# Kernel tuning notes

Hardware: AMD Instinct MI355X
Metric: run time of the kernel (lower is better)

Reference implementation:

```python
import jax, jax.numpy as jnp
import numpy as np

N_NODES = 100000
N_EDGES = 1000000
IN_DIM = 64
HID_DIM = 64


def _gcn_conv(x, W, b, rows, cols, deg_inv_sqrt):
    # x: [N, Fin] -> [N, Fout]; rows/cols already include self-loops
    xw = x @ W                                   # [N, Fout]
    norm = deg_inv_sqrt[rows] * deg_inv_sqrt[cols]  # [E+N]
    msg = xw[cols] * norm[:, None]               # gather + scale, [E+N, Fout]
    out = jax.ops.segment_sum(msg, rows, num_segments=x.shape[0])  # scatter-add
    return out + b


def _prelu(x, a):
    return jnp.where(x >= 0, x, a * x)


def _encode(x, edge_index, perm, W1, b1, prelu_a, W2, b2):
    N = x.shape[0]
    loops = jnp.arange(N, dtype=edge_index.dtype)
    rows = jnp.concatenate([edge_index[0], loops])
    cols = jnp.concatenate([edge_index[1], loops])
    deg = jax.ops.segment_sum(jnp.ones_like(rows, dtype=x.dtype), rows, num_segments=N)
    dis = jnp.where(deg > 0, jax.lax.rsqrt(deg), 0.0)

    def enc(feat):
        h = _gcn_conv(feat, W1, b1, rows, cols, dis)
        h = _prelu(h, prelu_a)
        return _gcn_conv(h, W2, b2, rows, cols, dis)

    positive = enc(x)
    negative = enc(x[perm])  # corruption: row permutation of features
    summary = jax.nn.sigmoid(positive.mean(axis=0))
    return positive, negative, summary


def setup_inputs() -> dict:
    key = jax.random.key(0)
    kx, ke, kp, k1, k2 = jax.random.split(key, 5)
    x = jax.random.normal(kx, (N_NODES, IN_DIM), dtype=jnp.float32)
    edge_index = jax.random.randint(ke, (2, N_EDGES), 0, N_NODES, dtype=jnp.int32)
    perm = jax.random.permutation(kp, N_NODES).astype(jnp.int32)
    s1 = 1.0 / np.sqrt(IN_DIM)
    s2 = 1.0 / np.sqrt(HID_DIM)
    W1 = jax.random.uniform(k1, (IN_DIM, HID_DIM), jnp.float32, -s1, s1)
    b1 = jnp.zeros((HID_DIM,), jnp.float32)
    W2 = jax.random.uniform(k2, (HID_DIM, HID_DIM), jnp.float32, -s2, s2)
    b2 = jnp.zeros((HID_DIM,), jnp.float32)
    prelu_a = jnp.float32(0.25)
    return {"x": x, "edge_index": edge_index, "perm": perm,
            "W1": W1, "b1": b1, "prelu_a": prelu_a, "W2": W2, "b2": b2}


def reference(x, edge_index, perm, W1, b1, prelu_a, W2, b2):
    return _encode(x, edge_index, perm, W1, b1, prelu_a, W2, b2)
```

## Files before the change

kernel.cpp:

```cpp
#include <hip/hip_runtime.h>
#include <hip/hip_fp16.h>
#include <math.h>

namespace {

constexpr int NN = 100000;
constexpr int NE = 1000000;
constexpr int D  = 64;

constexpr int RPB_LOG = 8;
constexpr int RPB = 1 << RPB_LOG;
constexpr int NBUK = (NN + RPB - 1) >> RPB_LOG;
constexpr int CAP = 4096;
constexpr int TILE = 8192;
constexpr int NTILES = (NE + TILE - 1) / TILE;
constexpr int EPT = TILE / 512;
constexpr int G1B = (NN / 16 + 7) / 8;
constexpr int SUMS = 256;

using ushort_t = unsigned short;
typedef __attribute__((ext_vector_type(8))) short short8;
typedef __attribute__((ext_vector_type(4))) float f32x4;

union FragU { uint4 v; short8 s; };

__device__ inline void split2(float f0, float f1, unsigned int& hi, unsigned int& lo) {
    unsigned int u0 = __float_as_uint(f0);
    unsigned int u1 = __float_as_uint(f1);
    hi = (u0 >> 16) | (u1 & 0xffff0000u);
    float l0 = f0 - __uint_as_float(u0 & 0xffff0000u);
    float l1 = f1 - __uint_as_float(u1 & 0xffff0000u);
    lo = (__float_as_uint(l0) >> 16) | (__float_as_uint(l1) & 0xffff0000u);
}

__device__ inline unsigned int packh(float a, float b) {
    union { __half2 h; unsigned int u; } cv;
    cv.h = __float22half2_rn(make_float2(a, b));
    return cv.u;
}

__device__ inline float2 h2f(unsigned int v) {
    union { unsigned int u; __half2 h; } cv;
    cv.u = v;
    return __half22float2(cv.h);
}

__device__ inline void build_wfrags(const float* __restrict__ W, int lane,
                                    FragU (&whi)[4][2], FragU (&wlo)[4][2]) {
#pragma unroll
    for (int ft = 0; ft < 4; ++ft) {
#pragma unroll
        for (int kt = 0; kt < 2; ++kt) {
            int m  = ft * 16 + (lane & 15);
            int k0 = kt * 32 + (lane >> 4) * 8;
            unsigned int hi0, lo0, hi1, lo1, hi2, lo2, hi3, lo3;
            split2(W[(k0 + 0) * 64 + m], W[(k0 + 1) * 64 + m], hi0, lo0);
            split2(W[(k0 + 2) * 64 + m], W[(k0 + 3) * 64 + m], hi1, lo1);
            split2(W[(k0 + 4) * 64 + m], W[(k0 + 5) * 64 + m], hi2, lo2);
            split2(W[(k0 + 6) * 64 + m], W[(k0 + 7) * 64 + m], hi3, lo3);
            whi[ft][kt].v = make_uint4(hi0, hi1, hi2, hi3);
            wlo[ft][kt].v = make_uint4(lo0, lo1, lo2, lo3);
        }
    }
}

__global__ void pre_k(const int* __restrict__ rows, const int* __restrict__ cols,
                      int* __restrict__ bcount, unsigned int* __restrict__ binned, int e,
                      const float* __restrict__ W1,
                      const float* __restrict__ x, const int* __restrict__ perm,
                      ushort_t* __restrict__ tPN) {
    __shared__ int gbase[NBUK];
    __shared__ int lofs[NBUK];
    int bid = blockIdx.x;

    if (bid >= NTILES) {
        int lane  = threadIdx.x & 63;
        int wtile = (bid - NTILES) * 8 + (threadIdx.x >> 6);
        if (wtile * 16 >= NN) return;
        int node = wtile * 16 + (lane & 15);
        int kg   = lane >> 4;

        FragU whi[4][2];
        FragU wlo[4][2];
        build_wfrags(W1, lane, whi, wlo);

        const float4* xr = (const float4*)x;
        size_t rbase = (size_t)node * 16 + (size_t)(kg * 2);
        int pnode = perm[node];
        size_t pbase = (size_t)pnode * 16 + (size_t)(kg * 2);
        f32x4 accP[4];
        f32x4 accN[4];
#pragma unroll
        for (int ft = 0; ft < 4; ++ft) {
            accP[ft] = f32x4{0.f, 0.f, 0.f, 0.f};
            accN[ft] = f32x4{0.f, 0.f, 0.f, 0.f};
        }
#pragma unroll
        for (int kt = 0; kt < 2; ++kt) {
            float4 a0 = xr[rbase + kt * 8];
            float4 a1 = xr[rbase + kt * 8 + 1];
            float4 g0 = xr[pbase + kt * 8];
            float4 g1 = xr[pbase + kt * 8 + 1];
            unsigned int h0, l0, h1, l1, h2, l2, h3, l3;
            split2(a0.x, a0.y, h0, l0);
            split2(a0.z, a0.w, h1, l1);
            split2(a1.x, a1.y, h2, l2);
            split2(a1.z, a1.w, h3, l3);
            FragU xhiP, xloP;
            xhiP.v = make_uint4(h0, h1, h2, h3);
            xloP.v = make_uint4(l0, l1, l2, l3);
            split2(g0.x, g0.y, h0, l0);
            split2(g0.z, g0.w, h1, l1);
            split2(g1.x, g1.y, h2, l2);
            split2(g1.z, g1.w, h3, l3);
            FragU xhiN, xloN;
            xhiN.v = make_uint4(h0, h1, h2, h3);
            xloN.v = make_uint4(l0, l1, l2, l3);
#pragma unroll
            for (int ft = 0; ft < 4; ++ft) {
                accP[ft] = __builtin_amdgcn_mfma_f32_16x16x32_bf16(whi[ft][kt].s, xhiP.s, accP[ft], 0, 0, 0);
                accP[ft] = __builtin_amdgcn_mfma_f32_16x16x32_bf16(whi[ft][kt].s, xloP.s, accP[ft], 0, 0, 0);
                accP[ft] = __builtin_amdgcn_mfma_f32_16x16x32_bf16(wlo[ft][kt].s, xhiP.s, accP[ft], 0, 0, 0);
                accN[ft] = __builtin_amdgcn_mfma_f32_16x16x32_bf16(whi[ft][kt].s, xhiN.s, accN[ft], 0, 0, 0);
                accN[ft] = __builtin_amdgcn_mfma_f32_16x16x32_bf16(whi[ft][kt].s, xloN.s, accN[ft], 0, 0, 0);
                accN[ft] = __builtin_amdgcn_mfma_f32_16x16x32_bf16(wlo[ft][kt].s, xhiN.s, accN[ft], 0, 0, 0);
            }
        }
        int fo = kg * 4;
        ushort_t* p = tPN + (size_t)node * 128;
#pragma unroll
        for (int ft = 0; ft < 4; ++ft) {
            uint2 up = make_uint2(packh(accP[ft][0], accP[ft][1]),
                                  packh(accP[ft][2], accP[ft][3]));
            *(uint2*)(p + ft * 16 + fo) = up;
            uint2 un = make_uint2(packh(accN[ft][0], accN[ft][1]),
                                  packh(accN[ft][2], accN[ft][3]));
            *(uint2*)(p + 64 + ft * 16 + fo) = un;
        }
        return;
    }

    int base = bid * TILE;
    for (int i = threadIdx.x; i < NBUK; i += blockDim.x) {
        lofs[i] = 0;
    }
    __syncthreads();
    unsigned int v[EPT];
    int bk[EPT];
    int lx[EPT];
#pragma unroll
    for (int j = 0; j < EPT; ++j) {
        int i = base + j * 512 + (int)threadIdx.x;
        if (i < e) {
            int r = rows[i];
            int c = cols[i];
            bk[j] = r >> RPB_LOG;
            v[j] = ((unsigned int)(r & (RPB - 1)) << 17) | (unsigned int)c;
            lx[j] = atomicAdd(&lofs[bk[j]], 1);
        } else {
            bk[j] = -1;
        }
    }
    __syncthreads();
    for (int b = threadIdx.x; b < NBUK; b += blockDim.x) {
        int h = lofs[b];
        gbase[b] = h ? atomicAdd(&bcount[b], h) : 0;
    }
    __syncthreads();
#pragma unroll
    for (int j = 0; j < EPT; ++j) {
        if (bk[j] >= 0) {
            int p = gbase[bk[j]] + lx[j];
            if (p < CAP) {
                binned[(size_t)bk[j] * CAP + p] = v[j];
            }
        }
    }
}

__global__ void bucket_sort_k(const unsigned int* __restrict__ binned,
                              const int* __restrict__ bcount,
                              int* __restrict__ scols, int* __restrict__ rowstart,
                              int* __restrict__ deg, float* __restrict__ dis) {
    __shared__ int lcur[RPB];
    __shared__ int srs[RPB];
    __shared__ int wsum[8];
    __shared__ int redpart[8];
    __shared__ int sbase;
    int b = blockIdx.x;
    int row0 = b << RPB_LOG;
    int nrows = min(RPB, NN - row0);
    int cnt = bcount[b];
    const unsigned int* src = binned + (size_t)b * CAP;
    int tid = threadIdx.x;
    int lane = tid & 63;
    int wid = tid >> 6;

    int bv = (tid < NBUK && tid < b) ? bcount[tid] : 0;
    int bs = bv;
#pragma unroll
    for (int off = 1; off < 64; off <<= 1) {
        bs += __shfl_xor(bs, off, 64);
    }
    if (lane == 0) redpart[wid] = bs;
    __syncthreads();
    if (tid == 0) {
        int t = 0;
        for (int w = 0; w < 8; ++w) t += redpart[w];
        sbase = t;
    }
    if (tid < RPB) {
        lcur[tid] = 0;
    }
    __syncthreads();
    int bb = sbase;

    for (int i = tid; i < cnt; i += blockDim.x) {
        atomicAdd(&lcur[src[i] >> 17], 1);
    }
    __syncthreads();
    int d = (tid < nrows) ? lcur[tid] : 0;
    int inc = d;
#pragma unroll
    for (int off = 1; off < 64; off <<= 1) {
        int t = __shfl_up(inc, off);
        if (lane >= off) inc += t;
    }
    if (lane == 63) wsum[wid] = inc;
    __syncthreads();
    int wpre = 0;
    for (int w = 0; w < wid; ++w) wpre += wsum[w];
    int gstart = bb + wpre + inc - d;
    if (tid < nrows) {
        rowstart[row0 + tid] = gstart;
        deg[row0 + tid] = d;
        dis[row0 + tid] = rsqrtf((float)(d + 1));
    }
    __syncthreads();
    if (tid < RPB) {
        srs[tid] = gstart;
        lcur[tid] = 0;
    }
    __syncthreads();
    for (int i = tid; i < cnt; i += blockDim.x) {
        unsigned int v = src[i];
        int rl = (int)(v >> 17);
        int pos = srs[rl] + atomicAdd(&lcur[rl], 1);
        scols[pos] = (int)(v & 0x1FFFFu);
    }
}

__global__ void agg_gemm_k(const ushort_t* __restrict__ tIn, ushort_t* __restrict__ tOut,
                           const float* __restrict__ dis,
                           const int* __restrict__ rowstart, const int* __restrict__ deg,
                           const int* __restrict__ scols,
                           const float* __restrict__ bias, const float* __restrict__ prelu_a,
                           const float* __restrict__ W2) {
    __shared__ float Hs[2][16][68];
    int tid = threadIdx.x;
    int lane = tid & 63;
    int wv = tid >> 6;
    int row0 = blockIdx.x * 16;
    int hl = lane & 31;
    int half = lane >> 5;
    size_t lofs = (size_t)(half * 64 + hl * 2);
    float aPr = *prelu_a;

    for (int rr = 0; rr < 4; ++rr) {
        int r = row0 + wv * 4 + rr;
        int rs   = __builtin_amdgcn_readfirstlane(r);
        int base = __builtin_amdgcn_readfirstlane(rowstart[rs]);
        int dg   = __builtin_amdgcn_readfirstlane(deg[rs]);
        float dr = dis[rs];
        unsigned int sv = *(const unsigned int*)(tIn + (size_t)rs * 128 + lofs);
        float2 fs = h2f(sv);
        float a0 = dr * fs.x;
        float a1 = dr * fs.y;
        int j = 0;
        for (; j + 4 <= dg; j += 4) {
            int c0 = scols[base + j];
            int c1 = scols[base + j + 1];
            int c2 = scols[base + j + 2];
            int c3 = scols[base + j + 3];
            float d0 = dis[c0];
            float d1 = dis[c1];
            float d2 = dis[c2];
            float d3 = dis[c3];
            unsigned int v0 = *(const unsigned int*)(tIn + (size_t)c0 * 128 + lofs);
            unsigned int v1 = *(const unsigned int*)(tIn + (size_t)c1 * 128 + lofs);
            unsigned int v2 = *(const unsigned int*)(tIn + (size_t)c2 * 128 + lofs);
            unsigned int v3 = *(const unsigned int*)(tIn + (size_t)c3 * 128 + lofs);
            float2 f0 = h2f(v0);
            float2 f1 = h2f(v1);
            float2 f2 = h2f(v2);
            float2 f3 = h2f(v3);
            a0 = fmaf(d0, f0.x, a0);
            a1 = fmaf(d0, f0.y, a1);
            a0 = fmaf(d1, f1.x, a0);
            a1 = fmaf(d1, f1.y, a1);
            a0 = fmaf(d2, f2.x, a0);
            a1 = fmaf(d2, f2.y, a1);
            a0 = fmaf(d3, f3.x, a0);
            a1 = fmaf(d3, f3.y, a1);
        }
        for (; j < dg; ++j) {
            int c = scols[base + j];
            float dc = dis[c];
            unsigned int v = *(const unsigned int*)(tIn + (size_t)c * 128 + lofs);
            float2 f = h2f(v);
            a0 = fmaf(dc, f.x, a0);
            a1 = fmaf(dc, f.y, a1);
        }
        float2 bv = *(const float2*)(bias + 2 * hl);
        float v0 = fmaf(dr, a0, bv.x);
        float v1 = fmaf(dr, a1, bv.y);
        v0 = v0 >= 0.f ? v0 : aPr * v0;
        v1 = v1 >= 0.f ? v1 : aPr * v1;
        int rl = wv * 4 + rr;
        Hs[half][rl][2 * hl]     = v0;
        Hs[half][rl][2 * hl + 1] = v1;
    }
    __syncthreads();

    int kg = lane >> 4;
    int nd = lane & 15;
    int hsel = wv >> 1;
    int ftb = (wv & 1) * 2;
    FragU whi[2][2];
    FragU wlo[2][2];
#pragma unroll
    for (int f2 = 0; f2 < 2; ++f2) {
#pragma unroll
        for (int kt = 0; kt < 2; ++kt) {
            int m  = (ftb + f2) * 16 + (lane & 15);
            int k0 = kt * 32 + (lane >> 4) * 8;
            unsigned int hi0, lo0, hi1, lo1, hi2, lo2, hi3, lo3;
            split2(W2[(k0 + 0) * 64 + m], W2[(k0 + 1) * 64 + m], hi0, lo0);
            split2(W2[(k0 + 2) * 64 + m], W2[(k0 + 3) * 64 + m], hi1, lo1);
            split2(W2[(k0 + 4) * 64 + m], W2[(k0 + 5) * 64 + m], hi2, lo2);
            split2(W2[(k0 + 6) * 64 + m], W2[(k0 + 7) * 64 + m], hi3, lo3);
            whi[f2][kt].v = make_uint4(hi0, hi1, hi2, hi3);
            wlo[f2][kt].v = make_uint4(lo0, lo1, lo2, lo3);
        }
    }
    f32x4 acc[2];
    acc[0] = f32x4{0.f, 0.f, 0.f, 0.f};
    acc[1] = f32x4{0.f, 0.f, 0.f, 0.f};
#pragma unroll
    for (int kt = 0; kt < 2; ++kt) {
        float4 a0 = *(const float4*)&Hs[hsel][nd][kt * 32 + kg * 8];
        float4 a1 = *(const float4*)&Hs[hsel][nd][kt * 32 + kg * 8 + 4];
        unsigned int h0, l0, h1, l1, h2, l2, h3, l3;
        split2(a0.x, a0.y, h0, l0);
        split2(a0.z, a0.w, h1, l1);
        split2(a1.x, a1.y, h2, l2);
        split2(a1.z, a1.w, h3, l3);
        FragU xhi, xlo;
        xhi.v = make_uint4(h0, h1, h2, h3);
        xlo.v = make_uint4(l0, l1, l2, l3);
#pragma unroll
        for (int f2 = 0; f2 < 2; ++f2) {
            acc[f2] = __builtin_amdgcn_mfma_f32_16x16x32_bf16(whi[f2][kt].s, xhi.s, acc[f2], 0, 0, 0);
            acc[f2] = __builtin_amdgcn_mfma_f32_16x16x32_bf16(whi[f2][kt].s, xlo.s, acc[f2], 0, 0, 0);
            acc[f2] = __builtin_amdgcn_mfma_f32_16x16x32_bf16(wlo[f2][kt].s, xhi.s, acc[f2], 0, 0, 0);
        }
    }
    float s = dis[row0 + nd];
    ushort_t* p = tOut + (size_t)(row0 + nd) * 128 + hsel * 64;
    int fo = kg * 4;
#pragma unroll
    for (int f2 = 0; f2 < 2; ++f2) {
        uint2 u = make_uint2(packh(s * acc[f2][0], s * acc[f2][1]),
                             packh(s * acc[f2][2], s * acc[f2][3]));
        *(uint2*)(p + (ftb + f2) * 16 + fo) = u;
    }
}

__global__ void agg_dual_k(const ushort_t* __restrict__ tPN,
                           float* __restrict__ dstP, float* __restrict__ dstN,
                           const float* __restrict__ dis,
                           const int* __restrict__ rowstart, const int* __restrict__ deg,
                           const int* __restrict__ scols,
                           const float* __restrict__ bias,
                           float* __restrict__ acc2, int n) {
    __shared__ float red[4][64];
    int lane = threadIdx.x & 63;
    int hl = lane & 31;
    int half = lane >> 5;
    int wv = threadIdx.x >> 6;
    int r = blockIdx.x * (blockDim.x >> 6) + wv;
    float v0 = 0.f;
    float v1 = 0.f;
    if (r < n) {
        int rs   = __builtin_amdgcn_readfirstlane(r);
        int base = __builtin_amdgcn_readfirstlane(rowstart[rs]);
        int dg   = __builtin_amdgcn_readfirstlane(deg[rs]);
        float dr = dis[rs];
        size_t lofs = (size_t)(half * 64 + hl * 2);
        unsigned int sv = *(const unsigned int*)(tPN + (size_t)rs * 128 + lofs);
        float2 fs = h2f(sv);
        float a0 = fs.x;
        float a1 = fs.y;
        int j = 0;
        for (; j + 4 <= dg; j += 4) {
            int c0 = scols[base + j];
            int c1 = scols[base + j + 1];
            int c2 = scols[base + j + 2];
            int c3 = scols[base + j + 3];
            unsigned int u0 = *(const unsigned int*)(tPN + (size_t)c0 * 128 + lofs);
            unsigned int u1 = *(const unsigned int*)(tPN + (size_t)c1 * 128 + lofs);
            unsigned int u2 = *(const unsigned int*)(tPN + (size_t)c2 * 128 + lofs);
            unsigned int u3 = *(const unsigned int*)(tPN + (size_t)c3 * 128 + lofs);
            float2 f0 = h2f(u0);
            float2 f1 = h2f(u1);
            float2 f2 = h2f(u2);
            float2 f3 = h2f(u3);
            a0 += f0.x + f1.x + f2.x + f3.x;
            a1 += f0.y + f1.y + f2.y + f3.y;
        }
        for (; j < dg; ++j) {
            int c = scols[base + j];
            unsigned int u = *(const unsigned int*)(tPN + (size_t)c * 128 + lofs);
            float2 f = h2f(u);
            a0 += f.x;
            a1 += f.y;
        }
        float2 bv = *(const float2*)(bias + 2 * hl);
        v0 = fmaf(dr, a0, bv.x);
        v1 = fmaf(dr, a1, bv.y);
        float* dst = half ? dstN : dstP;
        *(float2*)(dst + (size_t)rs * D + 2 * hl) = float2{v0, v1};
    }
    if (half == 0) {
        red[wv][2 * hl]     = v0;
        red[wv][2 * hl + 1] = v1;
    }
    __syncthreads();
    if (threadIdx.x < 64) {
        float t = (red[0][threadIdx.x] + red[1][threadIdx.x]) +
                  (red[2][threadIdx.x] + red[3][threadIdx.x]);
        atomicAdd(&acc2[((blockIdx.x & (SUMS - 1)) << 6) + threadIdx.x], t);
    }
}

__global__ void summary_final_k(const float* __restrict__ acc2, float* __restrict__ out, int n) {
    __shared__ float red[4][64];
    int f = threadIdx.x & 63;
    int g = threadIdx.x >> 6;
    float t = 0.f;
#pragma unroll
    for (int k = 0; k < SUMS / 4; ++k) {
        t += acc2[((g + 4 * k) << 6) + f];
    }
    red[g][f] = t;
    __syncthreads();
    if (threadIdx.x < 64) {
        float m = (red[0][f] + red[1][f] + red[2][f] + red[3][f]) / (float)n;
        out[f] = 1.f / (1.f + expf(-m));
    }
}

}

extern "C" void kernel_launch(void* const* d_in, const int* in_sizes, int n_in,
                              void* d_out, int out_size, void* d_ws, size_t ws_size,
                              hipStream_t stream) {
    (void)in_sizes; (void)n_in; (void)out_size; (void)ws_size;
    const float* x       = (const float*)d_in[0];
    const int*   ei      = (const int*)  d_in[1];
    const int*   perm    = (const int*)  d_in[2];
    const float* W1      = (const float*)d_in[3];
    const float* b1      = (const float*)d_in[4];
    const float* prelu_a = (const float*)d_in[5];
    const float* W2      = (const float*)d_in[6];
    const float* b2      = (const float*)d_in[7];

    float* outP = (float*)d_out;
    float* outN = outP + (size_t)NN * D;
    float* outS = outN + (size_t)NN * D;

    const int* erows = ei;
    const int* ecols = ei + NE;

    char* ws = (char*)d_ws;
    size_t off = 0;
    auto alloc = [&](size_t bytes) {
        void* p = ws + off;
        off = (off + bytes + 255) & ~(size_t)255;
        return p;
    };
    int*      deg      = (int*)     alloc((size_t)NN * 4);
    float*    dis      = (float*)   alloc((size_t)NN * 4);
    int*      rowstart = (int*)     alloc((size_t)NN * 4);
    int*      bcount   = (int*)     alloc((size_t)NBUK * 4);
    float*    acc2     = (float*)   alloc((size_t)SUMS * D * 4);
    unsigned int* binned = (unsigned int*)alloc((size_t)NBUK * CAP * 4);
    int*      scols    = (int*)     alloc((size_t)NE * 4);
    ushort_t* tPN      = (ushort_t*)alloc((size_t)NN * 128 * 2);
    ushort_t* tPN2     = (ushort_t*)alloc((size_t)NN * 128 * 2);

    hipMemsetAsync(bcount, 0,
                   (size_t)((char*)acc2 - (char*)bcount) + (size_t)SUMS * D * 4, stream);

    pre_k<<<NTILES + G1B, 512, 0, stream>>>(erows, ecols, bcount, binned, NE,
                                            W1, x, perm, tPN);
    bucket_sort_k<<<NBUK, 512, 0, stream>>>(binned, bcount, scols, rowstart, deg, dis);

    agg_gemm_k<<<NN / 16, 256, 0, stream>>>(tPN, tPN2, dis, rowstart, deg, scols,
                                            b1, prelu_a, W2);

    agg_dual_k<<<(NN + 3) / 4, 256, 0, stream>>>(tPN2, outP, outN, dis, rowstart, deg,
                                                 scols, b2, acc2, NN);

    summary_final_k<<<1, 256, 0, stream>>>(acc2, outS, NN);
}
```

Measured before the change: 232.5 us.

## Interleave four rows per wave in aggregation loops and precompute W2 fragments

Both aggregation kernels now have each wave process its four rows together in a single loop over the maximum degree. Each step issues 16 independent gathers at once, padding rows that have run out of edges with the self index and a zero weight. This raises memory-level parallelism for the latency-bound gathers, at the cost of wasted loads whenever row degrees differ within a wave. Separately, an extra block in pre_k splits W2 into hi/lo bf16 MFMA fragments once and stores them in a workspace buffer. agg_gemm_k loads these fragments instead of rebuilding them in every block, and agg_dual_k now handles 16 rows per block.

After: 232.0 us. About the same (-0.2%).

```diff
diff --git a/kernel.cpp b/kernel.cpp
--- a/kernel.cpp
+++ b/kernel.cpp
@@ -66,16 +66,17 @@
 
 __global__ void pre_k(const int* __restrict__ rows, const int* __restrict__ cols,
                       int* __restrict__ bcount, unsigned int* __restrict__ binned, int e,
-                      const float* __restrict__ W1,
+                      const float* __restrict__ W1, const float* __restrict__ W2,
+                      uint4* __restrict__ fb,
                       const float* __restrict__ x, const int* __restrict__ perm,
                       ushort_t* __restrict__ tPN) {
     __shared__ int gbase[NBUK];
     __shared__ int lofs[NBUK];
     int bid = blockIdx.x;
 
-    if (bid >= NTILES) {
+    if (bid > NTILES) {
         int lane  = threadIdx.x & 63;
-        int wtile = (bid - NTILES) * 8 + (threadIdx.x >> 6);
+        int wtile = (bid - NTILES - 1) * 8 + (threadIdx.x >> 6);
         if (wtile * 16 >= NN) return;
         int node = wtile * 16 + (lane & 15);
         int kg   = lane >> 4;
@@ -140,6 +141,26 @@
         return;
     }
 
+    if (bid == NTILES) {
+        int lane = threadIdx.x;
+        if (lane < 64) {
+            for (int ft = 0; ft < 4; ++ft) {
+                for (int kt = 0; kt < 2; ++kt) {
+                    int m  = ft * 16 + (lane & 15);
+                    int k0 = kt * 32 + (lane >> 4) * 8;
+                    unsigned int hi0, lo0, hi1, lo1, hi2, lo2, hi3, lo3;
+                    split2(W2[(k0 + 0) * 64 + m], W2[(k0 + 1) * 64 + m], hi0, lo0);
+                    split2(W2[(k0 + 2) * 64 + m], W2[(k0 + 3) * 64 + m], hi1, lo1);
+                    split2(W2[(k0 + 4) * 64 + m], W2[(k0 + 5) * 64 + m], hi2, lo2);
+                    split2(W2[(k0 + 6) * 64 + m], W2[(k0 + 7) * 64 + m], hi3, lo3);
+                    fb[((ft * 2 + kt) * 2 + 0) * 64 + lane] = make_uint4(hi0, hi1, hi2, hi3);
+                    fb[((ft * 2 + kt) * 2 + 1) * 64 + lane] = make_uint4(lo0, lo1, lo2, lo3);
+                }
+            }
+        }
+        return;
+    }
+
     int base = bid * TILE;
     for (int i = threadIdx.x; i < NBUK; i += blockDim.x) {
         lofs[i] = 0;
@@ -255,7 +276,7 @@
                            const int* __restrict__ rowstart, const int* __restrict__ deg,
                            const int* __restrict__ scols,
                            const float* __restrict__ bias, const float* __restrict__ prelu_a,
-                           const float* __restrict__ W2) {
+                           const uint4* __restrict__ wf) {
     __shared__ float Hs[2][16][68];
     int tid = threadIdx.x;
     int lane = tid & 63;
@@ -266,57 +287,66 @@
     size_t lofs = (size_t)(half * 64 + hl * 2);
     float aPr = *prelu_a;
 
-    for (int rr = 0; rr < 4; ++rr) {
-        int r = row0 + wv * 4 + rr;
-        int rs   = __builtin_amdgcn_readfirstlane(r);
-        int base = __builtin_amdgcn_readfirstlane(rowstart[rs]);
-        int dg   = __builtin_amdgcn_readfirstlane(deg[rs]);
+    int rsA[4];
+    int baA[4];
+    int dgA[4];
+    float drA[4];
+    float a0A[4];
+    float a1A[4];
+#pragma unroll
+    for (int q = 0; q < 4; ++q) {
+        int r = row0 + wv * 4 + q;
+        int rs = __builtin_amdgcn_readfirstlane(r);
+        rsA[q] = rs;
+        baA[q] = __builtin_amdgcn_readfirstlane(rowstart[rs]);
+        dgA[q] = __builtin_amdgcn_readfirstlane(deg[rs]);
         float dr = dis[rs];
+        drA[q] = dr;
         unsigned int sv = *(const unsigned int*)(tIn + (size_t)rs * 128 + lofs);
         float2 fs = h2f(sv);
-        float a0 = dr * fs.x;
-        float a1 = dr * fs.y;
-        int j = 0;
-        for (; j + 4 <= dg; j += 4) {
-            int c0 = scols[base + j];
-            int c1 = scols[base + j + 1];
-            int c2 = scols[base + j + 2];
-            int c3 = scols[base + j + 3];
-            float d0 = dis[c0];
-            float d1 = dis[c1];
-            float d2 = dis[c2];
-            float d3 = dis[c3];
-            unsigned int v0 = *(const unsigned int*)(tIn + (size_t)c0 * 128 + lofs);
-            unsigned int v1 = *(const unsigned int*)(tIn + (size_t)c1 * 128 + lofs);
-            unsigned int v2 = *(const unsigned int*)(tIn + (size_t)c2 * 128 + lofs);
-            unsigned int v3 = *(const unsigned int*)(tIn + (size_t)c3 * 128 + lofs);
-            float2 f0 = h2f(v0);
-            float2 f1 = h2f(v1);
-            float2 f2 = h2f(v2);
-            float2 f3 = h2f(v3);
-            a0 = fmaf(d0, f0.x, a0);
-            a1 = fmaf(d0, f0.y, a1);
-            a0 = fmaf(d1, f1.x, a0);
-            a1 = fmaf(d1, f1.y, a1);
-            a0 = fmaf(d2, f2.x, a0);
-            a1 = fmaf(d2, f2.y, a1);
-            a0 = fmaf(d3, f3.x, a0);
-            a1 = fmaf(d3, f3.y, a1);
-        }
-        for (; j < dg; ++j) {
-            int c = scols[base + j];
-            float dc = dis[c];
-            unsigned int v = *(const unsigned int*)(tIn + (size_t)c * 128 + lofs);
-            float2 f = h2f(v);
-            a0 = fmaf(dc, f.x, a0);
-            a1 = fmaf(dc, f.y, a1);
-        }
+        a0A[q] = dr * fs.x;
+        a1A[q] = dr * fs.y;
+    }
+    int maxdg = max(max(dgA[0], dgA[1]), max(dgA[2], dgA[3]));
+    for (int j = 0; j < maxdg; j += 4) {
+        unsigned int vv[4][4];
+        float dd[4][4];
+#pragma unroll
+        for (int q = 0; q < 4; ++q) {
+            int bq = baA[q];
+            int dq = dgA[q];
+            int rq = rsA[q];
+            int c0 = (j     < dq) ? scols[bq + j]     : rq;
+            int c1 = (j + 1 < dq) ? scols[bq + j + 1] : rq;
+            int c2 = (j + 2 < dq) ? scols[bq + j + 2] : rq;
+            int c3 = (j + 3 < dq) ? scols[bq + j + 3] : rq;
+            dd[q][0] = (j     < dq) ? dis[c0] : 0.f;
+            dd[q][1] = (j + 1 < dq) ? dis[c1] : 0.f;
+            dd[q][2] = (j + 2 < dq) ? dis[c2] : 0.f;
+            dd[q][3] = (j + 3 < dq) ? dis[c3] : 0.f;
+            vv[q][0] = *(const unsigned int*)(tIn + (size_t)c0 * 128 + lofs);
+            vv[q][1] = *(const unsigned int*)(tIn + (size_t)c1 * 128 + lofs);
+            vv[q][2] = *(const unsigned int*)(tIn + (size_t)c2 * 128 + lofs);
+            vv[q][3] = *(const unsigned int*)(tIn + (size_t)c3 * 128 + lofs);
+        }
+#pragma unroll
+        for (int q = 0; q < 4; ++q) {
+#pragma unroll
+            for (int s = 0; s < 4; ++s) {
+                float2 f = h2f(vv[q][s]);
+                a0A[q] = fmaf(dd[q][s], f.x, a0A[q]);
+                a1A[q] = fmaf(dd[q][s], f.y, a1A[q]);
+            }
+        }
+    }
+#pragma unroll
+    for (int q = 0; q < 4; ++q) {
         float2 bv = *(const float2*)(bias + 2 * hl);
-        float v0 = fmaf(dr, a0, bv.x);
-        float v1 = fmaf(dr, a1, bv.y);
+        float v0 = fmaf(drA[q], a0A[q], bv.x);
+        float v1 = fmaf(drA[q], a1A[q], bv.y);
         v0 = v0 >= 0.f ? v0 : aPr * v0;
         v1 = v1 >= 0.f ? v1 : aPr * v1;
-        int rl = wv * 4 + rr;
+        int rl = wv * 4 + q;
         Hs[half][rl][2 * hl]     = v0;
         Hs[half][rl][2 * hl + 1] = v1;
     }
@@ -332,15 +362,8 @@
     for (int f2 = 0; f2 < 2; ++f2) {
 #pragma unroll
         for (int kt = 0; kt < 2; ++kt) {
-            int m  = (ftb + f2) * 16 + (lane & 15);
-            int k0 = kt * 32 + (lane >> 4) * 8;
-            unsigned int hi0, lo0, hi1, lo1, hi2, lo2, hi3, lo3;
-            split2(W2[(k0 + 0) * 64 + m], W2[(k0 + 1) * 64 + m], hi0, lo0);
-            split2(W2[(k0 + 2) * 64 + m], W2[(k0 + 3) * 64 + m], hi1, lo1);
-            split2(W2[(k0 + 4) * 64 + m], W2[(k0 + 5) * 64 + m], hi2, lo2);
-            split2(W2[(k0 + 6) * 64 + m], W2[(k0 + 7) * 64 + m], hi3, lo3);
-            whi[f2][kt].v = make_uint4(hi0, hi1, hi2, hi3);
-            wlo[f2][kt].v = make_uint4(lo0, lo1, lo2, lo3);
+            whi[f2][kt].v = wf[(((ftb + f2) * 2 + kt) * 2 + 0) * 64 + lane];
+            wlo[f2][kt].v = wf[(((ftb + f2) * 2 + kt) * 2 + 1) * 64 + lane];
         }
     }
     f32x4 acc[2];
@@ -388,52 +411,75 @@
     int hl = lane & 31;
     int half = lane >> 5;
     int wv = threadIdx.x >> 6;
-    int r = blockIdx.x * (blockDim.x >> 6) + wv;
-    float v0 = 0.f;
-    float v1 = 0.f;
-    if (r < n) {
-        int rs   = __builtin_amdgcn_readfirstlane(r);
-        int base = __builtin_amdgcn_readfirstlane(rowstart[rs]);
-        int dg   = __builtin_amdgcn_readfirstlane(deg[rs]);
-        float dr = dis[rs];
-        size_t lofs = (size_t)(half * 64 + hl * 2);
+    int row0 = blockIdx.x * 16;
+    size_t lofs = (size_t)(half * 64 + hl * 2);
+    float2 bv = *(const float2*)(bias + 2 * hl);
+
+    int rsA[4];
+    int baA[4];
+    int dgA[4];
+    float drA[4];
+    float a0A[4];
+    float a1A[4];
+#pragma unroll
+    for (int q = 0; q < 4; ++q) {
+        int r = row0 + wv * 4 + q;
+        int rs = __builtin_amdgcn_readfirstlane(r);
+        rsA[q] = rs;
+        baA[q] = __builtin_amdgcn_readfirstlane(rowstart[rs]);
+        dgA[q] = __builtin_amdgcn_readfirstlane(deg[rs]);
+        drA[q] = dis[rs];
         unsigned int sv = *(const unsigned int*)(tPN + (size_t)rs * 128 + lofs);
         float2 fs = h2f(sv);
-        float a0 = fs.x;
-        float a1 = fs.y;
-        int j = 0;
-        for (; j + 4 <= dg; j += 4) {
-            int c0 = scols[base + j];
-            int c1 = scols[base + j + 1];
-            int c2 = scols[base + j + 2];
-            int c3 = scols[base + j + 3];
-            unsigned int u0 = *(const unsigned int*)(tPN + (size_t)c0 * 128 + lofs);
-            unsigned int u1 = *(const unsigned int*)(tPN + (size_t)c1 * 128 + lofs);
-            unsigned int u2 = *(const unsigned int*)(tPN + (size_t)c2 * 128 + lofs);
-            unsigned int u3 = *(const unsigned int*)(tPN + (size_t)c3 * 128 + lofs);
-            float2 f0 = h2f(u0);
-            float2 f1 = h2f(u1);
-            float2 f2 = h2f(u2);
-            float2 f3 = h2f(u3);
-            a0 += f0.x + f1.x + f2.x + f3.x;
-            a1 += f0.y + f1.y + f2.y + f3.y;
-        }
-        for (; j < dg; ++j) {
-            int c = scols[base + j];
-            unsigned int u = *(const unsigned int*)(tPN + (size_t)c * 128 + lofs);
-            float2 f = h2f(u);
-            a0 += f.x;
-            a1 += f.y;
-        }
-        float2 bv = *(const float2*)(bias + 2 * hl);
-        v0 = fmaf(dr, a0, bv.x);
-        v1 = fmaf(dr, a1, bv.y);
+        a0A[q] = fs.x;
+        a1A[q] = fs.y;
+    }
+    int maxdg = max(max(dgA[0], dgA[1]), max(dgA[2], dgA[3]));
+    for (int j = 0; j < maxdg; j += 4) {
+        unsigned int vv[4][4];
+        float ww[4][4];
+#pragma unroll
+        for (int q = 0; q < 4; ++q) {
+            int bq = baA[q];
+            int dq = dgA[q];
+            int rq = rsA[q];
+            int c0 = (j     < dq) ? scols[bq + j]     : rq;
+            int c1 = (j + 1 < dq) ? scols[bq + j + 1] : rq;
+            int c2 = (j + 2 < dq) ? scols[bq + j + 2] : rq;
+            int c3 = (j + 3 < dq) ? scols[bq + j + 3] : rq;
+            ww[q][0] = (j     < dq) ? 1.f : 0.f;
+            ww[q][1] = (j + 1 < dq) ? 1.f : 0.f;
+            ww[q][2] = (j + 2 < dq) ? 1.f : 0.f;
+            ww[q][3] = (j + 3 < dq) ? 1.f : 0.f;
+            vv[q][0] = *(const unsigned int*)(tPN + (size_t)c0 * 128 + lofs);
+            vv[q][1] = *(const unsigned int*)(tPN + (size_t)c1 * 128 + lofs);
+            vv[q][2] = *(const unsigned int*)(tPN + (size_t)c2 * 128 + lofs);
+            vv[q][3] = *(const unsigned int*)(tPN + (size_t)c3 * 128 + lofs);
+        }
+#pragma unroll
+        for (int q = 0; q < 4; ++q) {
+#pragma unroll
+            for (int s = 0; s < 4; ++s) {
+                float2 f = h2f(vv[q][s]);
+                a0A[q] = fmaf(ww[q][s], f.x, a0A[q]);
+                a1A[q] = fmaf(ww[q][s], f.y, a1A[q]);
+            }
+        }
+    }
+    float p0 = 0.f;
+    float p1 = 0.f;
+#pragma unroll
+    for (int q = 0; q < 4; ++q) {
+        float v0 = fmaf(drA[q], a0A[q], bv.x);
+        float v1 = fmaf(drA[q], a1A[q], bv.y);
         float* dst = half ? dstN : dstP;
-        *(float2*)(dst + (size_t)rs * D + 2 * hl) = float2{v0, v1};
+        *(float2*)(dst + (size_t)rsA[q] * D + 2 * hl) = float2{v0, v1};
+        p0 += v0;
+        p1 += v1;
     }
     if (half == 0) {
-        red[wv][2 * hl]     = v0;
-        red[wv][2 * hl + 1] = v1;
+        red[wv][2 * hl]     = p0;
+        red[wv][2 * hl + 1] = p1;
     }
     __syncthreads();
     if (threadIdx.x < 64) {
@@ -498,19 +544,20 @@
     int*      scols    = (int*)     alloc((size_t)NE * 4);
     ushort_t* tPN      = (ushort_t*)alloc((size_t)NN * 128 * 2);
     ushort_t* tPN2     = (ushort_t*)alloc((size_t)NN * 128 * 2);
+    uint4*    wfrag    = (uint4*)   alloc((size_t)1024 * 16);
 
     hipMemsetAsync(bcount, 0,
                    (size_t)((char*)acc2 - (char*)bcount) + (size_t)SUMS * D * 4, stream);
 
-    pre_k<<<NTILES + G1B, 512, 0, stream>>>(erows, ecols, bcount, binned, NE,
-                                            W1, x, perm, tPN);
+    pre_k<<<NTILES + 1 + G1B, 512, 0, stream>>>(erows, ecols, bcount, binned, NE,
+                                                W1, W2, wfrag, x, perm, tPN);
     bucket_sort_k<<<NBUK, 512, 0, stream>>>(binned, bcount, scols, rowstart, deg, dis);
 
     agg_gemm_k<<<NN / 16, 256, 0, stream>>>(tPN, tPN2, dis, rowstart, deg, scols,
-                                            b1, prelu_a, W2);
-
-    agg_dual_k<<<(NN + 3) / 4, 256, 0, stream>>>(tPN2, outP, outN, dis, rowstart, deg,
-                                                 scols, b2, acc2, NN);
+                                            b1, prelu_a, wfrag);
+
+    agg_dual_k<<<NN / 16, 256, 0, stream>>>(tPN2, outP, outN, dis, rowstart, deg,
+                                            scols, b2, acc2, NN);
 
     summary_final_k<<<1, 256, 0, stream>>>(acc2, outS, NN);
 }
```
